# Performance work log

Hardware: AMD Instinct MI355X
Metric: run time of the kernel (lower is better)

Reference implementation:

```python
import jax, jax.numpy as jnp
import numpy as np

B, S, D = 4, 2048, 1024

def setup_inputs() -> dict:
    key = jax.random.key(0)
    k1, k2, k3, k4 = jax.random.split(key, 4)
    scale = 1.0 / np.sqrt(D)  # roughly glorot-like magnitude for weights
    return {
        "inputs": jax.random.normal(k1, (B, S, D), dtype=jnp.float32),
        "W_query": jax.random.normal(k2, (D, D), dtype=jnp.float32) * scale,
        "W_key": jax.random.normal(k3, (D, D), dtype=jnp.float32) * scale,
        "W_value": jax.random.normal(k4, (D, D), dtype=jnp.float32) * scale,
    }

def reference(inputs, W_query, W_key, W_value):
    # QKV projections: [B,S,D] @ [D,D]
    q = jnp.einsum('bsd,de->bse', inputs, W_query)
    k = jnp.einsum('bsd,de->bse', inputs, W_key)
    v = jnp.einsum('bsd,de->bse', inputs, W_value)
    # Unscaled attention scores [B,S,S] (source applies no 1/sqrt(d))
    score = jnp.einsum('bqd,bkd->bqk', q, k)
    weights = jax.nn.softmax(score, axis=-1)
    context = jnp.einsum('bqk,bkd->bqd', weights, v)
    return context
```

## Files before the change

### kernel.cpp

```cpp
#include <hip/hip_runtime.h>
#include <math.h>


typedef __bf16 bf16;
typedef _Float16 f16;
typedef __bf16 bf16x8 __attribute__((ext_vector_type(8)));
typedef __bf16 bf16x4 __attribute__((ext_vector_type(4)));
typedef _Float16 f16x4 __attribute__((ext_vector_type(4)));
typedef _Float16 f16x8 __attribute__((ext_vector_type(8)));
typedef float  f32x4  __attribute__((ext_vector_type(4)));

template<typename E> struct vec8_of;
template<> struct vec8_of<bf16> { using type = bf16x8; };
template<> struct vec8_of<f16>  { using type = f16x8; };

__device__ inline f32x4 mfma16(bf16x8 a, bf16x8 b, f32x4 c) {
    return __builtin_amdgcn_mfma_f32_16x16x32_bf16(a, b, c, 0, 0, 0);
}
__device__ inline f32x4 mfma16(f16x8 a, f16x8 b, f32x4 c) {
    return __builtin_amdgcn_mfma_f32_16x16x32_f16(a, b, c, 0, 0, 0);
}

#define AS1 __attribute__((address_space(1)))
#define AS3 __attribute__((address_space(3)))

template<typename E>
__device__ inline void async_load16(const E* g, void* l) {
    __builtin_amdgcn_global_load_lds((const AS1 unsigned int*)g,
                                     (AS3 unsigned int*)l, 16, 0, 0);
}

#define SBAR()  do { __builtin_amdgcn_s_barrier(); __builtin_amdgcn_sched_barrier(0); } while (0)
#define WAITV(n) do { asm volatile("s_waitcnt vmcnt(" #n ")" ::: "memory"); __builtin_amdgcn_sched_barrier(0); } while (0)
#define WAITL() do { asm volatile("s_waitcnt lgkmcnt(0)" ::: "memory"); __builtin_amdgcn_sched_barrier(0); } while (0)

__device__ inline void xcd_swz(int nwg, int gx, int& bx, int& by) {
    const int flat = by * gx + bx;
    const int s = (flat & 7) * (nwg >> 3) + (flat >> 3);
    bx = s % gx;
    by = s / gx;
}

template<int OUT_MODE, int BMQ>
__device__ __forceinline__ void gemm_deep_body(
    char* __restrict__ smraw,
    const f16* __restrict__ A, const f16* __restrict__ B,
    float* __restrict__ Cf, f16* __restrict__ Ch,
    int K, int lda, int ldb, int ldc,
    long long sA, long long sB, long long sC,
    int bx, int by, int bz)
{
    constexpr int ACH   = BMQ * 8192;
    constexpr int BOFF  = 2 * ACH;
    constexpr int BUFSZ = 2 * ACH + 32768;
    constexpr int nI    = 4 * BMQ;

    A += (long long)bz * sA;
    B += (long long)bz * sB;

    const int tid  = threadIdx.x;
    const int lane = tid & 63;
    const int wave = tid >> 6;
    const int quad = lane >> 4;
    const int l16  = lane & 15;
    const int wm   = wave >> 2;
    const int wn   = wave & 3;

    const long long rowA0 = (long long)by * (BMQ * 128);
    const long long colB0 = (long long)bx * 256;

    const int line0 = tid >> 3;
    const int slog  = (tid & 7) ^ (line0 & 7);
    const int r0s   = line0 * 2 + (slog >> 2);
    const int c0s   = (slog & 3) * 8;

    const f16* aSrc0 = A + (rowA0 + r0s) * lda + c0s;
    const f16* aSrc1 = A + (rowA0 + 128 + r0s) * lda + c0s;
    const f16* bSrc0 = B + (colB0 + r0s) * ldb + c0s;
    const f16* bSrc1 = B + (colB0 + 128 + r0s) * ldb + c0s;

    const int nt = K >> 6;

    auto stageA = [&](int t, int kh) {
        char* dst = smraw + (t & 1) * BUFSZ + kh * ACH;
        const int k0 = t * 64 + kh * 32;
        async_load16(aSrc0 + k0, dst + tid * 16);
        if constexpr (BMQ == 2) async_load16(aSrc1 + k0, dst + 8192 + tid * 16);
    };
    auto stageB = [&](int t, int kh) {
        char* dst = smraw + (t & 1) * BUFSZ + BOFF + kh * 16384;
        const int k0 = t * 64 + kh * 32;
        async_load16(bSrc0 + k0, dst + tid * 16);
        async_load16(bSrc1 + k0, dst + 8192 + tid * 16);
    };

    const int h    = l16 >> 1;
    const int lofs = h * 128 + ((((l16 & 1) * 4 + quad) ^ h) << 4);
    const int aoff = wm * (ACH / 2) + lofs;
    const int boff = BOFF + wn * 4096 + lofs;

    f32x4 acc[nI][4];
#pragma unroll
    for (int i = 0; i < nI; i++)
#pragma unroll
        for (int j = 0; j < 4; j++) acc[i][j] = (f32x4){0.f, 0.f, 0.f, 0.f};

    stageA(0, 0); stageA(0, 1); stageB(0, 0); stageB(0, 1);
    WAITV(2);
    SBAR();

    for (int t = 0; t < nt; t++) {
        const char* buf = smraw + (t & 1) * BUFSZ;
        f16x8 av[nI], bv[2];

#pragma unroll
        for (int i = 0; i < nI; i++) av[i] = *(const f16x8*)(buf + aoff + i * 1024);
        bv[0] = *(const f16x8*)(buf + boff);
        bv[1] = *(const f16x8*)(buf + boff + 1024);
        if (t + 1 < nt) { stageA(t + 1, 0); stageA(t + 1, 1); }
        SBAR();
        WAITL();
        __builtin_amdgcn_s_setprio(1);
#pragma unroll
        for (int i = 0; i < nI; i++) {
            acc[i][0] = mfma16(av[i], bv[0], acc[i][0]);
            acc[i][1] = mfma16(av[i], bv[1], acc[i][1]);
        }
        __builtin_amdgcn_s_setprio(0);
        SBAR();

        bv[0] = *(const f16x8*)(buf + boff + 2048);
        bv[1] = *(const f16x8*)(buf + boff + 3072);
        if (t + 1 < nt) { stageB(t + 1, 0); stageB(t + 1, 1); }
        SBAR();
        WAITL();
        __builtin_amdgcn_s_setprio(1);
#pragma unroll
        for (int i = 0; i < nI; i++) {
            acc[i][2] = mfma16(av[i], bv[0], acc[i][2]);
            acc[i][3] = mfma16(av[i], bv[1], acc[i][3]);
        }
        __builtin_amdgcn_s_setprio(0);
        if (t + 1 < nt) { if constexpr (BMQ == 2) WAITV(8); else WAITV(6); }
        else { WAITV(0); }
        SBAR();

#pragma unroll
        for (int i = 0; i < nI; i++) av[i] = *(const f16x8*)(buf + ACH + aoff + i * 1024);
        bv[0] = *(const f16x8*)(buf + 16384 + boff);
        bv[1] = *(const f16x8*)(buf + 16384 + boff + 1024);
        SBAR();
        WAITL();
        __builtin_amdgcn_s_setprio(1);
#pragma unroll
        for (int i = 0; i < nI; i++) {
            acc[i][0] = mfma16(av[i], bv[0], acc[i][0]);
            acc[i][1] = mfma16(av[i], bv[1], acc[i][1]);
        }
        __builtin_amdgcn_s_setprio(0);
        SBAR();

        bv[0] = *(const f16x8*)(buf + 16384 + boff + 2048);
        bv[1] = *(const f16x8*)(buf + 16384 + boff + 3072);
        SBAR();
        WAITL();
        __builtin_amdgcn_s_setprio(1);
#pragma unroll
        for (int i = 0; i < nI; i++) {
            acc[i][2] = mfma16(av[i], bv[0], acc[i][2]);
            acc[i][3] = mfma16(av[i], bv[1], acc[i][3]);
        }
        __builtin_amdgcn_s_setprio(0);
        if (t + 1 < nt) { WAITV(2); } else { WAITV(0); }
        SBAR();
    }

    if constexpr (OUT_MODE == 2) {
        auto tr = (f16(*)[72])smraw;
        const int batch = (int)(rowA0 >> 11);
        const long long rib = rowA0 & 2047;
        const int c  = tid >> 1;
        const int r0 = (tid & 1) << 5;
#pragma unroll
        for (int h2 = 0; h2 < 2; h2++)
#pragma unroll
            for (int iq = 0; iq < 2; iq++) {
                __syncthreads();
                if (wm == h2) {
#pragma unroll
                    for (int i2 = 0; i2 < 4; i2++)
#pragma unroll
                        for (int j = 0; j < 4; j++)
#pragma unroll
                            for (int e = 0; e < 4; e++)
                                tr[wn * 64 + j * 16 + l16][i2 * 16 + quad * 4 + e] =
                                    (f16)acc[iq * 4 + i2][j][e];
                }
                __syncthreads();
                f16* vt = Ch + (long long)batch * 1024 * 2048 +
                          (long long)(colB0 + c) * ldc + rib + h2 * 128 + iq * 64 + r0;
#pragma unroll
                for (int u = 0; u < 32; u += 8)
                    *(f16x8*)(vt + u) = *(const f16x8*)&tr[c][r0 + u];
            }
        return;
    }

    const long long cOff = (long long)bz * sC +
                           (rowA0 + wm * (BMQ * 64) + quad * 4) * (long long)ldc +
                           colB0 + wn * 64 + l16;
#pragma unroll
    for (int i = 0; i < nI; i++)
#pragma unroll
        for (int e = 0; e < 4; e++) {
            const long long ro = cOff + (long long)(i * 16 + e) * ldc;
            if (OUT_MODE == 0) {
                float* rp = Cf + ro;
#pragma unroll
                for (int j = 0; j < 4; j++) rp[j * 16] = acc[i][j][e];
            } else {
                f16* rp = Ch + ro;
#pragma unroll
                for (int j = 0; j < 4; j++) rp[j * 16] = (f16)acc[i][j][e];
            }
        }
}

__global__ __launch_bounds__(512, 2) void tv8d(
    const f16* __restrict__ Xf, const f16* __restrict__ Mt_f,
    const f16* __restrict__ Wvt_f, f16* __restrict__ T, f16* __restrict__ Vt)
{
    extern __shared__ char smraw[];
    int bx = blockIdx.x, by = blockIdx.y;
    xcd_swz(256, 8, bx, by);
    if (bx < 4)
        gemm_deep_body<1, 2>(smraw, Xf, Mt_f, nullptr, T, 1024, 1024, 1024, 1024,
                             0, 0, 0, bx, by, 0);
    else
        gemm_deep_body<2, 2>(smraw, Xf, Wvt_f, nullptr, Vt, 1024, 1024, 1024, 2048,
                             0, 0, 0, bx - 4, by, 0);
}

template<int OUT_MODE, int BMQ>
__global__ __launch_bounds__(512, 2) void gemmd_k(
    const f16* __restrict__ A, const f16* __restrict__ B,
    float* __restrict__ Cf, f16* __restrict__ Ch,
    int K, int lda, int ldb, int ldc,
    long long sA, long long sB, long long sC)
{
    extern __shared__ char smraw[];
    int bx = blockIdx.x, by = blockIdx.y;
    xcd_swz(gridDim.x * gridDim.y, gridDim.x, bx, by);
    gemm_deep_body<OUT_MODE, BMQ>(smraw, A, B, Cf, Ch, K, lda, ldb, ldc,
                                  sA, sB, sC, bx, by, blockIdx.z);
}

template<int OUT_MODE, int BMQ>
__device__ __forceinline__ void gemm8_body(
    char* __restrict__ smraw,
    const f16* __restrict__ A, const f16* __restrict__ B,
    float* __restrict__ Cf, f16* __restrict__ Ch,
    int K, int lda, int ldb, int ldc,
    long long sA, long long sB, long long sC,
    int bx, int by, int bz)
{
    constexpr int B0OFF = BMQ * 8192;
    constexpr int B1OFF = B0OFF + 8192;
    constexpr int BUFSZ = B0OFF + 16384;

    A += (long long)bz * sA;
    B += (long long)bz * sB;

    const int tid  = threadIdx.x;
    const int lane = tid & 63;
    const int wave = tid >> 6;
    const int quad = lane >> 4;
    const int l16  = lane & 15;
    const int wm   = wave >> 2;
    const int wn   = wave & 3;

    const long long rowA0 = (long long)by * (BMQ * 128);
    const long long colB0 = (long long)bx * 256;

    const int line0 = tid >> 3;
    const int slog  = (tid & 7) ^ (line0 & 7);
    const int aRow0 = line0 * 2 + (slog >> 2);
    const int aCol0 = (slog & 3) * 8;
    const int bRow  = ((aRow0 >> 5) << 6) + (aRow0 & 31);

    const f16* aSrc0 = A + (rowA0 + aRow0) * lda + aCol0;
    const f16* aSrc1 = A + (rowA0 + 128 + aRow0) * lda + aCol0;
    const f16* b0Src = B + (colB0 + bRow) * ldb + aCol0;
    const f16* b1Src = b0Src + 32LL * ldb;

    const int dA0 = tid * 16, dA1 = 8192 + tid * 16;

    const int nt = K >> 5;

    auto stageA = [&](int t) {
        char* buf = smraw + (t & 1) * BUFSZ;
        async_load16(aSrc0 + t * 32, buf + dA0);
        if (BMQ == 2) async_load16(aSrc1 + t * 32, buf + dA1);
    };
    auto stageB0 = [&](int t) {
        char* buf = smraw + (t & 1) * BUFSZ;
        async_load16(b0Src + t * 32, buf + B0OFF + dA0);
    };
    auto stageB1 = [&](int t) {
        char* buf = smraw + (t & 1) * BUFSZ;
        async_load16(b1Src + t * 32, buf + B1OFF + dA0);
    };

    const int h    = l16 >> 1;
    const int lofs = h * 128 + ((((l16 & 1) * 4 + quad) ^ h) << 4);
    const int aoff = wm * (BMQ * 4096) + lofs;
    const int boff = wn * 2048 + lofs;

    f32x4 acc[4 * BMQ][4];
#pragma unroll
    for (int i = 0; i < 4 * BMQ; i++)
#pragma unroll
        for (int j = 0; j < 4; j++) acc[i][j] = (f32x4){0.f, 0.f, 0.f, 0.f};

    stageA(0); stageB0(0); stageB1(0);
    stageA(1); stageB0(1);
    if constexpr (BMQ == 2) WAITV(4); else WAITV(3);
    SBAR();

    for (int t = 0; t < nt; t++) {
        const char* buf = smraw + (t & 1) * BUFSZ;
        f16x8 av[4 * BMQ], bv[2];

#pragma unroll
        for (int i = 0; i < 4 * BMQ; i++) av[i] = *(const f16x8*)(buf + aoff + i * 1024);
#pragma unroll
        for (int j = 0; j < 2; j++) bv[j] = *(const f16x8*)(buf + B0OFF + boff + j * 1024);
        if (t + 1 < nt) stageB1(t + 1);
        SBAR();
        WAITL();
        __builtin_amdgcn_s_setprio(1);
#pragma unroll
        for (int i = 0; i < 4 * BMQ; i++) {
            acc[i][0] = mfma16(av[i], bv[0], acc[i][0]);
            acc[i][1] = mfma16(av[i], bv[1], acc[i][1]);
        }
        __builtin_amdgcn_s_setprio(0);
        if (t + 1 < nt) { if constexpr (BMQ == 2) WAITV(4); else WAITV(3); }
        else WAITV(0);
        SBAR();

#pragma unroll
        for (int j = 0; j < 2; j++) bv[j] = *(const f16x8*)(buf + B1OFF + boff + j * 1024);
        if (t + 2 < nt) { stageA(t + 2); stageB0(t + 2); }
        SBAR();
        WAITL();
        __builtin_amdgcn_s_setprio(1);
#pragma unroll
        for (int i = 0; i < 4 * BMQ; i++) {
            acc[i][2] = mfma16(av[i], bv[0], acc[i][2]);
            acc[i][3] = mfma16(av[i], bv[1], acc[i][3]);
        }
        __builtin_amdgcn_s_setprio(0);
        if (t + 2 < nt) { if constexpr (BMQ == 2) WAITV(4); else WAITV(3); }
        else if (t + 1 < nt) WAITV(1);
        SBAR();
    }

    if constexpr (OUT_MODE == 2) {
        auto tr = (f16(*)[72])smraw;
        const int batch = (int)(rowA0 >> 11);
        const long long rib = rowA0 & 2047;
        const int c  = tid >> 1;
        const int r0 = (tid & 1) << 5;
#pragma unroll
        for (int h2 = 0; h2 < 2; h2++)
#pragma unroll
            for (int iq = 0; iq < 2; iq++) {
                __syncthreads();
                if (wm == h2) {
#pragma unroll
                    for (int i2 = 0; i2 < 4; i2++)
#pragma unroll
                        for (int j = 0; j < 4; j++)
#pragma unroll
                            for (int e = 0; e < 4; e++)
                                tr[wn * 64 + j * 16 + l16][i2 * 16 + quad * 4 + e] =
                                    (f16)acc[iq * 4 + i2][j][e];
                }
                __syncthreads();
                f16* vt = Ch + (long long)batch * 1024 * 2048 +
                          (long long)(colB0 + c) * ldc + rib + h2 * 128 + iq * 64 + r0;
#pragma unroll
                for (int u = 0; u < 32; u += 8)
                    *(f16x8*)(vt + u) = *(const f16x8*)&tr[c][r0 + u];
            }
        return;
    }

    const long long cOff = (long long)bz * sC +
                           (rowA0 + wm * (BMQ * 64) + quad * 4) * (long long)ldc +
                           colB0 + wn * 64 + l16;
#pragma unroll
    for (int i = 0; i < 4 * BMQ; i++)
#pragma unroll
        for (int e = 0; e < 4; e++) {
            const long long ro = cOff + (long long)(i * 16 + e) * ldc;
            if (OUT_MODE == 0) {
                float* rp = Cf + ro;
#pragma unroll
                for (int j = 0; j < 4; j++) rp[j * 16] = acc[i][j][e];
            } else {
                f16* rp = Ch + ro;
#pragma unroll
                for (int j = 0; j < 4; j++) rp[j * 16] = (f16)acc[i][j][e];
            }
        }
}

__global__ __launch_bounds__(512, 2) void tv8(
    const f16* __restrict__ Xf, const f16* __restrict__ Mt_f,
    const f16* __restrict__ Wvt_f, f16* __restrict__ T, f16* __restrict__ Vt)
{
    extern __shared__ char smraw[];
    int bx = blockIdx.x, by = blockIdx.y;
    xcd_swz(256, 8, bx, by);
    if (bx < 4)
        gemm8_body<1, 2>(smraw, Xf, Mt_f, nullptr, T, 1024, 1024, 1024, 1024,
                         0, 0, 0, bx, by, 0);
    else
        gemm8_body<2, 2>(smraw, Xf, Wvt_f, nullptr, Vt, 1024, 1024, 1024, 2048,
                         0, 0, 0, bx - 4, by, 0);
}

template<int OUT_MODE, int BMQ>
__global__ __launch_bounds__(512, 2) void gemm8_k(
    const f16* __restrict__ A, const f16* __restrict__ B,
    float* __restrict__ Cf, f16* __restrict__ Ch,
    int K, int lda, int ldb, int ldc,
    long long sA, long long sB, long long sC)
{
    extern __shared__ char smraw[];
    int bx = blockIdx.x, by = blockIdx.y;
    xcd_swz(gridDim.x * gridDim.y, gridDim.x, bx, by);
    gemm8_body<OUT_MODE, BMQ>(smraw, A, B, Cf, Ch, K, lda, ldb, ldc, sA, sB, sC,
                              bx, by, blockIdx.z);
}

template<typename E, bool SPLIT, int OUT_MODE, int BK>
__device__ __forceinline__ void gemm_body(
    char* __restrict__ smraw,
    const E* __restrict__ Ahi, const E* __restrict__ Alo,
    const E* __restrict__ Bhi, const E* __restrict__ Blo,
    float* __restrict__ Cf, f16* __restrict__ Ch,
    int K, int lda, int ldb, int ldc,
    long long sA, long long sB, long long sC,
    int bx, int by, int bz)
{
    using vec8 = typename vec8_of<E>::type;
    constexpr int TILE_BYTES = 128 * BK * (int)sizeof(E);
    constexpr int CPW = (TILE_BYTES / 1024) / 4;
    constexpr int SPR = (BK * (int)sizeof(E)) / 16;

    Ahi += (long long)bz * sA;
    Bhi += (long long)bz * sB;
    if (SPLIT) { Alo += (long long)bz * sA; Blo += (long long)bz * sB; }

    const int tid  = threadIdx.x;
    const int lane = tid & 63;
    const int wave = tid >> 6;
    const int quad = lane >> 4;
    const int l16  = lane & 15;
    const int wm   = (wave >> 1) * 64;
    const int wn   = (wave & 1) * 64;

    const long long rowA0 = (long long)by * 128;
    const long long colB0 = (long long)bx * 128;

    auto swz = [](int r) -> int { return (SPR == 8) ? (r & 7) : ((r >> 1) & 3); };

    int ofs[CPW], rr[CPW], cc8[CPW];
#pragma unroll
    for (int u = 0; u < CPW; u++) {
        ofs[u] = (wave * CPW + u) * 1024 + lane * 16;
        const int s = ofs[u] >> 4;
        rr[u]  = s / SPR;
        cc8[u] = (s & (SPR - 1)) ^ swz(rr[u]);
    }

    f32x4 acc[4][4];
#pragma unroll
    for (int i = 0; i < 4; i++)
#pragma unroll
        for (int j = 0; j < 4; j++) acc[i][j] = (f32x4){0.f, 0.f, 0.f, 0.f};

    for (int k0 = 0; k0 < K; k0 += BK) {
#pragma unroll
        for (int u = 0; u < CPW; u++) {
            async_load16(Ahi + (rowA0 + rr[u]) * lda + k0 + cc8[u] * 8, smraw + 0 * TILE_BYTES + ofs[u]);
            async_load16(Bhi + (colB0 + rr[u]) * ldb + k0 + cc8[u] * 8, smraw + 1 * TILE_BYTES + ofs[u]);
            if (SPLIT) {
                async_load16(Alo + (rowA0 + rr[u]) * lda + k0 + cc8[u] * 8, smraw + 2 * TILE_BYTES + ofs[u]);
                async_load16(Blo + (colB0 + rr[u]) * ldb + k0 + cc8[u] * 8, smraw + 3 * TILE_BYTES + ofs[u]);
            }
        }
        __syncthreads();

#pragma unroll
        for (int kh = 0; kh < BK / 32; kh++) {
            const int kc8 = kh * 4 + quad;
            vec8 a_hi[4], b_hi[4], a_lo[4], b_lo[4];
#pragma unroll
            for (int i = 0; i < 4; i++) {
                const int ra = wm + i * 16 + l16;
                const int rb = wn + i * 16 + l16;
                const int oa = ra * (SPR * 16) + ((kc8 ^ swz(ra)) << 4);
                const int ob = rb * (SPR * 16) + ((kc8 ^ swz(rb)) << 4);
                a_hi[i] = *(const vec8*)(smraw + 0 * TILE_BYTES + oa);
                b_hi[i] = *(const vec8*)(smraw + 1 * TILE_BYTES + ob);
                if (SPLIT) {
                    a_lo[i] = *(const vec8*)(smraw + 2 * TILE_BYTES + oa);
                    b_lo[i] = *(const vec8*)(smraw + 3 * TILE_BYTES + ob);
                }
            }
#pragma unroll
            for (int i = 0; i < 4; i++)
#pragma unroll
                for (int j = 0; j < 4; j++) {
                    acc[i][j] = mfma16(a_hi[i], b_hi[j], acc[i][j]);
                    if (SPLIT) {
                        acc[i][j] = mfma16(a_hi[i], b_lo[j], acc[i][j]);
                        acc[i][j] = mfma16(a_lo[i], b_hi[j], acc[i][j]);
                    }
                }
        }
        __syncthreads();
    }

    const long long cOff = (long long)bz * sC +
                           (rowA0 + wm + quad * 4) * (long long)ldc + colB0 + wn + l16;
#pragma unroll
    for (int i = 0; i < 4; i++)
#pragma unroll
        for (int e = 0; e < 4; e++) {
            const long long ro = cOff + (i * 16 + e) * ldc;
            if (OUT_MODE == 0) {
                float* rp = Cf + ro;
#pragma unroll
                for (int j = 0; j < 4; j++) rp[j * 16] = acc[i][j][e];
            } else {
                f16* rp = Ch + ro;
#pragma unroll
                for (int j = 0; j < 4; j++) rp[j * 16] = (f16)acc[i][j][e];
            }
        }
}

template<typename E, bool SPLIT, int OUT_MODE, int BK>
__global__ __launch_bounds__(256) void gemm_bt(
    const E* __restrict__ Ahi, const E* __restrict__ Alo,
    const E* __restrict__ Bhi, const E* __restrict__ Blo,
    float* __restrict__ Cf, f16* __restrict__ Ch,
    int K, int lda, int ldb, int ldc,
    long long sA, long long sB, long long sC)
{
    extern __shared__ char smraw[];
    gemm_body<E, SPLIT, OUT_MODE, BK>(smraw, Ahi, Alo, Bhi, Blo, Cf, Ch,
                                      K, lda, ldb, ldc, sA, sB, sC,
                                      blockIdx.x, blockIdx.y, blockIdx.z);
}

__global__ __launch_bounds__(256) void prep_all(
    const float4* __restrict__ X, f16* __restrict__ Xf,
    const float* __restrict__ Wq, const float* __restrict__ Wk, const float* __restrict__ Wv,
    bf16* __restrict__ Wq_h, bf16* __restrict__ Wq_l,
    bf16* __restrict__ Wk_h, bf16* __restrict__ Wk_l,
    f16* __restrict__ Wvt_f)
{
    int b = blockIdx.x;
    if (b < 8192) {
        long long i = (long long)b * 256 + threadIdx.x;
        float4 v = X[i];
        f16x4 fv = {(f16)v.x, (f16)v.y, (f16)v.z, (f16)v.w};
        *(f16x4*)(Xf + 4 * i) = fv;
    } else if (b < 10240) {
        const int b2 = b - 8192;
        const float4* W = (const float4*)(b2 < 1024 ? Wq : Wk);
        bf16* hh = b2 < 1024 ? Wq_h : Wk_h;
        bf16* ll = b2 < 1024 ? Wq_l : Wk_l;
        long long i = (long long)(b2 & 1023) * 256 + threadIdx.x;
        float4 v = W[i];
        bf16 a0 = (bf16)v.x, a1 = (bf16)v.y, a2 = (bf16)v.z, a3 = (bf16)v.w;
        bf16x4 hv = {a0, a1, a2, a3};
        bf16x4 lv = {(bf16)(v.x - (float)a0), (bf16)(v.y - (float)a1),
                     (bf16)(v.z - (float)a2), (bf16)(v.w - (float)a3)};
        *(bf16x4*)(hh + 4 * i) = hv;
        *(bf16x4*)(ll + 4 * i) = lv;
    } else {
        const int b3 = b - 10240;
        __shared__ float t[32][33];
        const int bx = (b3 & 31) * 32, by = (b3 >> 5) * 32;
        const int tx = threadIdx.x & 31, ty = threadIdx.x >> 5;
#pragma unroll
        for (int i = 0; i < 32; i += 8)
            t[ty + i][tx] = Wv[(long long)(by + ty + i) * 1024 + bx + tx];
        __syncthreads();
#pragma unroll
        for (int i = 0; i < 32; i += 8) {
            long long o = (long long)(bx + ty + i) * 1024 + by + tx;
            Wvt_f[o] = (f16)t[tx][ty + i];
        }
    }
}

__global__ __launch_bounds__(256) void softmax_f16(const float* __restrict__ S,
                                                   f16* __restrict__ P, int n)
{
    const long long row = blockIdx.x;
    const float4* p = (const float4*)(S + row * (long long)n);
    f16* q = P + row * (long long)n;
    const int tid = threadIdx.x;
    const int wv = tid >> 6, lane = tid & 63;

    float4 va = p[tid], vb = p[tid + 256];
    float v[8] = {va.x, va.y, va.z, va.w, vb.x, vb.y, vb.z, vb.w};
    float m = -3.4e38f;
#pragma unroll
    for (int i = 0; i < 8; i++) m = fmaxf(m, v[i]);
#pragma unroll
    for (int off = 32; off > 0; off >>= 1) m = fmaxf(m, __shfl_xor(m, off, 64));

    __shared__ float red[4];
    if (lane == 0) red[wv] = m;
    __syncthreads();
    m = fmaxf(fmaxf(red[0], red[1]), fmaxf(red[2], red[3]));

    float s = 0.f;
#pragma unroll
    for (int i = 0; i < 8; i++) { v[i] = __expf(v[i] - m); s += v[i]; }
#pragma unroll
    for (int off = 32; off > 0; off >>= 1) s += __shfl_xor(s, off, 64);
    __syncthreads();
    if (lane == 0) red[wv] = s;
    __syncthreads();
    s = red[0] + red[1] + red[2] + red[3];

    const float inv = 1.0f / s;
    f16x4 o0 = {(f16)(v[0] * inv), (f16)(v[1] * inv), (f16)(v[2] * inv), (f16)(v[3] * inv)};
    f16x4 o1 = {(f16)(v[4] * inv), (f16)(v[5] * inv), (f16)(v[6] * inv), (f16)(v[7] * inv)};
    *(f16x4*)(q + tid * 4) = o0;
    *(f16x4*)(q + 1024 + tid * 4) = o1;
}

extern "C" void kernel_launch(void* const* d_in, const int* in_sizes, int n_in,
                              void* d_out, int out_size, void* d_ws, size_t ws_size,
                              hipStream_t stream) {
    const float* X  = (const float*)d_in[0];
    const float* Wq = (const float*)d_in[1];
    const float* Wk = (const float*)d_in[2];
    const float* Wv = (const float*)d_in[3];
    float* out = (float*)d_out;

    char* w = (char*)d_ws;
    const long long MB = 1024LL * 1024;
    f16*  Xf    = (f16*) (w + 0 * MB);
    bf16* Wq_h  = (bf16*)(w + 16 * MB);
    bf16* Wq_l  = (bf16*)(w + 18 * MB);
    bf16* Wk_h  = (bf16*)(w + 20 * MB);
    bf16* Wk_l  = (bf16*)(w + 22 * MB);
    f16*  Wvt_f = (f16*) (w + 24 * MB);
    f16*  Mt_f  = (f16*) (w + 26 * MB);
    f16*  T     = (f16*) (w + 28 * MB);
    f16*  Vt    = (f16*) (w + 44 * MB);
    float* Sc   = (float*)(w + 60 * MB);
    f16*  P     = (f16*) (w + 124 * MB);

    static int deep_ok = -1;
    if (deep_ok < 0) {
        auto* pSc = gemmd_k<0, 2>;
        auto* pPv = gemmd_k<0, 1>;
        hipError_t e1 = hipFuncSetAttribute(
            reinterpret_cast<const void*>(tv8d),
            hipFuncAttributeMaxDynamicSharedMemorySize, 131072);
        hipError_t e2 = hipFuncSetAttribute(
            reinterpret_cast<const void*>(pSc),
            hipFuncAttributeMaxDynamicSharedMemorySize, 131072);
        hipError_t e3 = hipFuncSetAttribute(
            reinterpret_cast<const void*>(pPv),
            hipFuncAttributeMaxDynamicSharedMemorySize, 98304);
        deep_ok = (e1 == hipSuccess && e2 == hipSuccess && e3 == hipSuccess) ? 1 : 0;
    }

    dim3 blk(256);

    prep_all<<<dim3(11264), blk, 0, stream>>>(
        (const float4*)X, Xf, Wq, Wk, Wv, Wq_h, Wq_l, Wk_h, Wk_l, Wvt_f);

    gemm_bt<bf16, true, 1, 32><<<dim3(8, 8, 1), blk, 32768, stream>>>(
        Wk_h, Wk_l, Wq_h, Wq_l, nullptr, Mt_f,
        1024, 1024, 1024, 1024, 0, 0, 0);

    if (deep_ok) {
        tv8d<<<dim3(8, 32), dim3(512), 131072, stream>>>(Xf, Mt_f, Wvt_f, T, Vt);
        gemmd_k<0, 2><<<dim3(8, 8, 4), dim3(512), 131072, stream>>>(
            T, Xf, Sc, nullptr, 1024, 1024, 1024, 2048,
            2048LL * 1024, 2048LL * 1024, 2048LL * 2048);
        softmax_f16<<<dim3(4 * 2048), blk, 0, stream>>>(Sc, P, 2048);
        gemmd_k<0, 1><<<dim3(4, 16, 4), dim3(512), 98304, stream>>>(
            P, Vt, out, nullptr, 2048, 2048, 2048, 1024,
            2048LL * 2048, 1024LL * 2048, 2048LL * 1024);
    } else {
        tv8<<<dim3(8, 32), dim3(512), 65536, stream>>>(Xf, Mt_f, Wvt_f, T, Vt);
        gemm8_k<0, 2><<<dim3(8, 8, 4), dim3(512), 65536, stream>>>(
            T, Xf, Sc, nullptr, 1024, 1024, 1024, 2048,
            2048LL * 1024, 2048LL * 1024, 2048LL * 2048);
        softmax_f16<<<dim3(4 * 2048), blk, 0, stream>>>(Sc, P, 2048);
        gemm8_k<0, 1><<<dim3(4, 16, 4), dim3(512), 49152, stream>>>(
            P, Vt, out, nullptr, 2048, 2048, 2048, 1024,
            2048LL * 2048, 1024LL * 2048, 2048LL * 1024);
    }
}
```

Baseline: 275.2 us.

## Fuse whole attention pipeline into one cooperative persistent kernel with grid barriers

Replaces the chain of separate launches (prep, weight-product GEMM, projection GEMMs, score GEMM, softmax, PV GEMM) with a single cooperative kernel of 256 persistent blocks. The stages are separated by a software grid barrier built from an atomic counter. The aim is to remove per-launch overhead and the idle tail between kernels. In exchange it adds barrier spin cost and loses the per-kernel XCD swizzle. The small Mt GEMM is also computed redundantly by both 256-thread halves of each 512-thread block, and the unused gemm8 fallback path is removed.

```diff
diff --git a/kernel.cpp b/kernel.cpp
--- a/kernel.cpp
+++ b/kernel.cpp
@@ -39,6 +39,18 @@
     const int s = (flat & 7) * (nwg >> 3) + (flat >> 3);
     bx = s % gx;
     by = s / gx;
+}
+
+__device__ inline void gbar(unsigned* bar, unsigned target) {
+    __syncthreads();
+    if (threadIdx.x == 0) {
+        __threadfence();
+        atomicAdd(bar, 1u);
+        while (__hip_atomic_load(bar, __ATOMIC_RELAXED, __HIP_MEMORY_SCOPE_AGENT) < target)
+            __builtin_amdgcn_s_sleep(32);
+    }
+    __syncthreads();
+    __threadfence();
 }
 
 template<int OUT_MODE, int BMQ>
@@ -226,226 +238,6 @@
         }
 }
 
-__global__ __launch_bounds__(512, 2) void tv8d(
-    const f16* __restrict__ Xf, const f16* __restrict__ Mt_f,
-    const f16* __restrict__ Wvt_f, f16* __restrict__ T, f16* __restrict__ Vt)
-{
-    extern __shared__ char smraw[];
-    int bx = blockIdx.x, by = blockIdx.y;
-    xcd_swz(256, 8, bx, by);
-    if (bx < 4)
-        gemm_deep_body<1, 2>(smraw, Xf, Mt_f, nullptr, T, 1024, 1024, 1024, 1024,
-                             0, 0, 0, bx, by, 0);
-    else
-        gemm_deep_body<2, 2>(smraw, Xf, Wvt_f, nullptr, Vt, 1024, 1024, 1024, 2048,
-                             0, 0, 0, bx - 4, by, 0);
-}
-
-template<int OUT_MODE, int BMQ>
-__global__ __launch_bounds__(512, 2) void gemmd_k(
-    const f16* __restrict__ A, const f16* __restrict__ B,
-    float* __restrict__ Cf, f16* __restrict__ Ch,
-    int K, int lda, int ldb, int ldc,
-    long long sA, long long sB, long long sC)
-{
-    extern __shared__ char smraw[];
-    int bx = blockIdx.x, by = blockIdx.y;
-    xcd_swz(gridDim.x * gridDim.y, gridDim.x, bx, by);
-    gemm_deep_body<OUT_MODE, BMQ>(smraw, A, B, Cf, Ch, K, lda, ldb, ldc,
-                                  sA, sB, sC, bx, by, blockIdx.z);
-}
-
-template<int OUT_MODE, int BMQ>
-__device__ __forceinline__ void gemm8_body(
-    char* __restrict__ smraw,
-    const f16* __restrict__ A, const f16* __restrict__ B,
-    float* __restrict__ Cf, f16* __restrict__ Ch,
-    int K, int lda, int ldb, int ldc,
-    long long sA, long long sB, long long sC,
-    int bx, int by, int bz)
-{
-    constexpr int B0OFF = BMQ * 8192;
-    constexpr int B1OFF = B0OFF + 8192;
-    constexpr int BUFSZ = B0OFF + 16384;
-
-    A += (long long)bz * sA;
-    B += (long long)bz * sB;
-
-    const int tid  = threadIdx.x;
-    const int lane = tid & 63;
-    const int wave = tid >> 6;
-    const int quad = lane >> 4;
-    const int l16  = lane & 15;
-    const int wm   = wave >> 2;
-    const int wn   = wave & 3;
-
-    const long long rowA0 = (long long)by * (BMQ * 128);
-    const long long colB0 = (long long)bx * 256;
-
-    const int line0 = tid >> 3;
-    const int slog  = (tid & 7) ^ (line0 & 7);
-    const int aRow0 = line0 * 2 + (slog >> 2);
-    const int aCol0 = (slog & 3) * 8;
-    const int bRow  = ((aRow0 >> 5) << 6) + (aRow0 & 31);
-
-    const f16* aSrc0 = A + (rowA0 + aRow0) * lda + aCol0;
-    const f16* aSrc1 = A + (rowA0 + 128 + aRow0) * lda + aCol0;
-    const f16* b0Src = B + (colB0 + bRow) * ldb + aCol0;
-    const f16* b1Src = b0Src + 32LL * ldb;
-
-    const int dA0 = tid * 16, dA1 = 8192 + tid * 16;
-
-    const int nt = K >> 5;
-
-    auto stageA = [&](int t) {
-        char* buf = smraw + (t & 1) * BUFSZ;
-        async_load16(aSrc0 + t * 32, buf + dA0);
-        if (BMQ == 2) async_load16(aSrc1 + t * 32, buf + dA1);
-    };
-    auto stageB0 = [&](int t) {
-        char* buf = smraw + (t & 1) * BUFSZ;
-        async_load16(b0Src + t * 32, buf + B0OFF + dA0);
-    };
-    auto stageB1 = [&](int t) {
-        char* buf = smraw + (t & 1) * BUFSZ;
-        async_load16(b1Src + t * 32, buf + B1OFF + dA0);
-    };
-
-    const int h    = l16 >> 1;
-    const int lofs = h * 128 + ((((l16 & 1) * 4 + quad) ^ h) << 4);
-    const int aoff = wm * (BMQ * 4096) + lofs;
-    const int boff = wn * 2048 + lofs;
-
-    f32x4 acc[4 * BMQ][4];
-#pragma unroll
-    for (int i = 0; i < 4 * BMQ; i++)
-#pragma unroll
-        for (int j = 0; j < 4; j++) acc[i][j] = (f32x4){0.f, 0.f, 0.f, 0.f};
-
-    stageA(0); stageB0(0); stageB1(0);
-    stageA(1); stageB0(1);
-    if constexpr (BMQ == 2) WAITV(4); else WAITV(3);
-    SBAR();
-
-    for (int t = 0; t < nt; t++) {
-        const char* buf = smraw + (t & 1) * BUFSZ;
-        f16x8 av[4 * BMQ], bv[2];
-
-#pragma unroll
-        for (int i = 0; i < 4 * BMQ; i++) av[i] = *(const f16x8*)(buf + aoff + i * 1024);
-#pragma unroll
-        for (int j = 0; j < 2; j++) bv[j] = *(const f16x8*)(buf + B0OFF + boff + j * 1024);
-        if (t + 1 < nt) stageB1(t + 1);
-        SBAR();
-        WAITL();
-        __builtin_amdgcn_s_setprio(1);
-#pragma unroll
-        for (int i = 0; i < 4 * BMQ; i++) {
-            acc[i][0] = mfma16(av[i], bv[0], acc[i][0]);
-            acc[i][1] = mfma16(av[i], bv[1], acc[i][1]);
-        }
-        __builtin_amdgcn_s_setprio(0);
-        if (t + 1 < nt) { if constexpr (BMQ == 2) WAITV(4); else WAITV(3); }
-        else WAITV(0);
-        SBAR();
-
-#pragma unroll
-        for (int j = 0; j < 2; j++) bv[j] = *(const f16x8*)(buf + B1OFF + boff + j * 1024);
-        if (t + 2 < nt) { stageA(t + 2); stageB0(t + 2); }
-        SBAR();
-        WAITL();
-        __builtin_amdgcn_s_setprio(1);
-#pragma unroll
-        for (int i = 0; i < 4 * BMQ; i++) {
-            acc[i][2] = mfma16(av[i], bv[0], acc[i][2]);
-            acc[i][3] = mfma16(av[i], bv[1], acc[i][3]);
-        }
-        __builtin_amdgcn_s_setprio(0);
-        if (t + 2 < nt) { if constexpr (BMQ == 2) WAITV(4); else WAITV(3); }
-        else if (t + 1 < nt) WAITV(1);
-        SBAR();
-    }
-
-    if constexpr (OUT_MODE == 2) {
-        auto tr = (f16(*)[72])smraw;
-        const int batch = (int)(rowA0 >> 11);
-        const long long rib = rowA0 & 2047;
-        const int c  = tid >> 1;
-        const int r0 = (tid & 1) << 5;
-#pragma unroll
-        for (int h2 = 0; h2 < 2; h2++)
-#pragma unroll
-            for (int iq = 0; iq < 2; iq++) {
-                __syncthreads();
-                if (wm == h2) {
-#pragma unroll
-                    for (int i2 = 0; i2 < 4; i2++)
-#pragma unroll
-                        for (int j = 0; j < 4; j++)
-#pragma unroll
-                            for (int e = 0; e < 4; e++)
-                                tr[wn * 64 + j * 16 + l16][i2 * 16 + quad * 4 + e] =
-                                    (f16)acc[iq * 4 + i2][j][e];
-                }
-                __syncthreads();
-                f16* vt = Ch + (long long)batch * 1024 * 2048 +
-                          (long long)(colB0 + c) * ldc + rib + h2 * 128 + iq * 64 + r0;
-#pragma unroll
-                for (int u = 0; u < 32; u += 8)
-                    *(f16x8*)(vt + u) = *(const f16x8*)&tr[c][r0 + u];
-            }
-        return;
-    }
-
-    const long long cOff = (long long)bz * sC +
-                           (rowA0 + wm * (BMQ * 64) + quad * 4) * (long long)ldc +
-                           colB0 + wn * 64 + l16;
-#pragma unroll
-    for (int i = 0; i < 4 * BMQ; i++)
-#pragma unroll
-        for (int e = 0; e < 4; e++) {
-            const long long ro = cOff + (long long)(i * 16 + e) * ldc;
-            if (OUT_MODE == 0) {
-                float* rp = Cf + ro;
-#pragma unroll
-                for (int j = 0; j < 4; j++) rp[j * 16] = acc[i][j][e];
-            } else {
-                f16* rp = Ch + ro;
-#pragma unroll
-                for (int j = 0; j < 4; j++) rp[j * 16] = (f16)acc[i][j][e];
-            }
-        }
-}
-
-__global__ __launch_bounds__(512, 2) void tv8(
-    const f16* __restrict__ Xf, const f16* __restrict__ Mt_f,
-    const f16* __restrict__ Wvt_f, f16* __restrict__ T, f16* __restrict__ Vt)
-{
-    extern __shared__ char smraw[];
-    int bx = blockIdx.x, by = blockIdx.y;
-    xcd_swz(256, 8, bx, by);
-    if (bx < 4)
-        gemm8_body<1, 2>(smraw, Xf, Mt_f, nullptr, T, 1024, 1024, 1024, 1024,
-                         0, 0, 0, bx, by, 0);
-    else
-        gemm8_body<2, 2>(smraw, Xf, Wvt_f, nullptr, Vt, 1024, 1024, 1024, 2048,
-                         0, 0, 0, bx - 4, by, 0);
-}
-
-template<int OUT_MODE, int BMQ>
-__global__ __launch_bounds__(512, 2) void gemm8_k(
-    const f16* __restrict__ A, const f16* __restrict__ B,
-    float* __restrict__ Cf, f16* __restrict__ Ch,
-    int K, int lda, int ldb, int ldc,
-    long long sA, long long sB, long long sC)
-{
-    extern __shared__ char smraw[];
-    int bx = blockIdx.x, by = blockIdx.y;
-    xcd_swz(gridDim.x * gridDim.y, gridDim.x, bx, by);
-    gemm8_body<OUT_MODE, BMQ>(smraw, A, B, Cf, Ch, K, lda, ldb, ldc, sA, sB, sC,
-                              bx, by, blockIdx.z);
-}
-
 template<typename E, bool SPLIT, int OUT_MODE, int BK>
 __device__ __forceinline__ void gemm_body(
     char* __restrict__ smraw,
@@ -454,7 +246,7 @@
     float* __restrict__ Cf, f16* __restrict__ Ch,
     int K, int lda, int ldb, int ldc,
     long long sA, long long sB, long long sC,
-    int bx, int by, int bz)
+    int bx, int by, int bz, int tid)
 {
     using vec8 = typename vec8_of<E>::type;
     constexpr int TILE_BYTES = 128 * BK * (int)sizeof(E);
@@ -465,7 +257,6 @@
     Bhi += (long long)bz * sB;
     if (SPLIT) { Alo += (long long)bz * sA; Blo += (long long)bz * sB; }
 
-    const int tid  = threadIdx.x;
     const int lane = tid & 63;
     const int wave = tid >> 6;
     const int quad = lane >> 4;
@@ -555,6 +346,162 @@
         }
 }
 
+__device__ __forceinline__ void softmax512(const float* __restrict__ S,
+                                           f16* __restrict__ P,
+                                           long long row, int tid, char* smraw)
+{
+    float* red = (float*)smraw;
+    const float4* p = (const float4*)(S + row * 2048);
+    f16* q = P + row * 2048;
+    const int wv = tid >> 6, lane = tid & 63;
+
+    float4 va = p[tid];
+    float m = fmaxf(fmaxf(va.x, va.y), fmaxf(va.z, va.w));
+#pragma unroll
+    for (int off = 32; off > 0; off >>= 1) m = fmaxf(m, __shfl_xor(m, off, 64));
+    __syncthreads();
+    if (lane == 0) red[wv] = m;
+    __syncthreads();
+    m = fmaxf(fmaxf(fmaxf(red[0], red[1]), fmaxf(red[2], red[3])),
+              fmaxf(fmaxf(red[4], red[5]), fmaxf(red[6], red[7])));
+
+    float e0 = __expf(va.x - m), e1 = __expf(va.y - m);
+    float e2 = __expf(va.z - m), e3 = __expf(va.w - m);
+    float s = (e0 + e1) + (e2 + e3);
+#pragma unroll
+    for (int off = 32; off > 0; off >>= 1) s += __shfl_xor(s, off, 64);
+    __syncthreads();
+    if (lane == 0) red[wv] = s;
+    __syncthreads();
+    s = ((red[0] + red[1]) + (red[2] + red[3])) +
+        ((red[4] + red[5]) + (red[6] + red[7]));
+
+    const float inv = 1.0f / s;
+    f16x4 o = {(f16)(e0 * inv), (f16)(e1 * inv), (f16)(e2 * inv), (f16)(e3 * inv)};
+    *(f16x4*)(q + tid * 4) = o;
+}
+
+__global__ __launch_bounds__(512, 2) void mega(
+    const float* __restrict__ X, const float* __restrict__ Wq,
+    const float* __restrict__ Wk, const float* __restrict__ Wv,
+    float* __restrict__ out, f16* __restrict__ Xf,
+    bf16* __restrict__ Wq_h, bf16* __restrict__ Wq_l,
+    bf16* __restrict__ Wk_h, bf16* __restrict__ Wk_l,
+    f16* __restrict__ Wvt_f, f16* __restrict__ Mt_f,
+    f16* __restrict__ T, f16* __restrict__ Vt,
+    float* __restrict__ Sc, f16* __restrict__ P, unsigned* bar)
+{
+    extern __shared__ char smraw[];
+    const int b = blockIdx.x, tid = threadIdx.x;
+
+    for (int u = b; u < 1536; u += 256) {
+        if (u < 1024) {
+            const float4* W = (const float4*)(u < 512 ? Wq : Wk);
+            bf16* hh = u < 512 ? Wq_h : Wk_h;
+            bf16* ll = u < 512 ? Wq_l : Wk_l;
+            long long i = (long long)(u & 511) * 512 + tid;
+            float4 v = W[i];
+            bf16 a0 = (bf16)v.x, a1 = (bf16)v.y, a2 = (bf16)v.z, a3 = (bf16)v.w;
+            bf16x4 hv = {a0, a1, a2, a3};
+            bf16x4 lv = {(bf16)(v.x - (float)a0), (bf16)(v.y - (float)a1),
+                         (bf16)(v.z - (float)a2), (bf16)(v.w - (float)a3)};
+            *(bf16x4*)(hh + 4 * i) = hv;
+            *(bf16x4*)(ll + 4 * i) = lv;
+        } else {
+            auto t = (float(*)[32][33])smraw;
+            const int tile = (u - 1024) * 2 + (tid >> 8);
+            const int sub = tid & 255;
+            const int bx = (tile & 31) * 32, by = (tile >> 5) * 32;
+            const int tx = sub & 31, ty = sub >> 5;
+            __syncthreads();
+#pragma unroll
+            for (int i = 0; i < 32; i += 8)
+                t[tid >> 8][ty + i][tx] = Wv[(long long)(by + ty + i) * 1024 + bx + tx];
+            __syncthreads();
+#pragma unroll
+            for (int i = 0; i < 32; i += 8) {
+                long long o = (long long)(bx + ty + i) * 1024 + by + tx;
+                Wvt_f[o] = (f16)t[tid >> 8][tx][ty + i];
+            }
+        }
+    }
+    gbar(bar, 256);
+
+    if (b < 64) {
+        gemm_body<bf16, true, 1, 32>(smraw, Wk_h, Wk_l, Wq_h, Wq_l,
+                                     nullptr, Mt_f, 1024, 1024, 1024, 1024,
+                                     0, 0, 0, b & 7, b >> 3, 0, tid & 255);
+    } else {
+        for (int u = b - 64; u < 4096; u += 192) {
+            long long i = (long long)u * 512 + tid;
+            float4 v = ((const float4*)X)[i];
+            f16x4 fv = {(f16)v.x, (f16)v.y, (f16)v.z, (f16)v.w};
+            *(f16x4*)(Xf + 4 * i) = fv;
+        }
+    }
+    gbar(bar, 512);
+
+    if (b < 128) {
+        const int by = (b & 7) * 4 + ((b >> 3) & 3), bx = b >> 5;
+        gemm_deep_body<1, 2>(smraw, Xf, Mt_f, nullptr, T, 1024, 1024, 1024, 1024,
+                             0, 0, 0, bx, by, 0);
+    } else {
+        const int b2 = b - 128;
+        const int by = (b2 & 7) * 4 + ((b2 >> 3) & 3), bx = b2 >> 5;
+        gemm_deep_body<2, 2>(smraw, Xf, Wvt_f, nullptr, Vt, 1024, 1024, 1024, 2048,
+                             0, 0, 0, bx, by, 0);
+    }
+    gbar(bar, 768);
+
+    {
+        const int rem = b & 63, bz = b >> 6;
+        const int by = rem & 7, bx = rem >> 3;
+        gemm_deep_body<0, 2>(smraw, T, Xf, Sc, nullptr, 1024, 1024, 1024, 2048,
+                             2048LL * 1024, 2048LL * 1024, 2048LL * 2048, bx, by, bz);
+    }
+    gbar(bar, 1024);
+
+    for (int r = 0; r < 32; r++)
+        softmax512(Sc, P, (long long)b * 32 + r, tid, smraw);
+    gbar(bar, 1280);
+
+    {
+        const int rem = b & 63, bz = b >> 6;
+        const int by = (rem & 7) * 2 + ((rem >> 3) & 1), bx = rem >> 4;
+        gemm_deep_body<0, 1>(smraw, P, Vt, out, nullptr, 2048, 2048, 2048, 1024,
+                             2048LL * 2048, 1024LL * 2048, 2048LL * 1024, bx, by, bz);
+    }
+}
+
+__global__ __launch_bounds__(512, 2) void tv8d(
+    const f16* __restrict__ Xf, const f16* __restrict__ Mt_f,
+    const f16* __restrict__ Wvt_f, f16* __restrict__ T, f16* __restrict__ Vt)
+{
+    extern __shared__ char smraw[];
+    int bx = blockIdx.x, by = blockIdx.y;
+    xcd_swz(256, 8, bx, by);
+    if (bx < 4)
+        gemm_deep_body<1, 2>(smraw, Xf, Mt_f, nullptr, T, 1024, 1024, 1024, 1024,
+                             0, 0, 0, bx, by, 0);
+    else
+        gemm_deep_body<2, 2>(smraw, Xf, Wvt_f, nullptr, Vt, 1024, 1024, 1024, 2048,
+                             0, 0, 0, bx - 4, by, 0);
+}
+
+template<int OUT_MODE, int BMQ>
+__global__ __launch_bounds__(512, 2) void gemmd_k(
+    const f16* __restrict__ A, const f16* __restrict__ B,
+    float* __restrict__ Cf, f16* __restrict__ Ch,
+    int K, int lda, int ldb, int ldc,
+    long long sA, long long sB, long long sC)
+{
+    extern __shared__ char smraw[];
+    int bx = blockIdx.x, by = blockIdx.y;
+    xcd_swz(gridDim.x * gridDim.y, gridDim.x, bx, by);
+    gemm_deep_body<OUT_MODE, BMQ>(smraw, A, B, Cf, Ch, K, lda, ldb, ldc,
+                                  sA, sB, sC, bx, by, blockIdx.z);
+}
+
 template<typename E, bool SPLIT, int OUT_MODE, int BK>
 __global__ __launch_bounds__(256) void gemm_bt(
     const E* __restrict__ Ahi, const E* __restrict__ Alo,
@@ -566,7 +513,8 @@
     extern __shared__ char smraw[];
     gemm_body<E, SPLIT, OUT_MODE, BK>(smraw, Ahi, Alo, Bhi, Blo, Cf, Ch,
                                       K, lda, ldb, ldc, sA, sB, sC,
-                                      blockIdx.x, blockIdx.y, blockIdx.z);
+                                      blockIdx.x, blockIdx.y, blockIdx.z,
+                                      threadIdx.x);
 }
 
 __global__ __launch_bounds__(256) void prep_all(
@@ -674,10 +622,13 @@
     float* Sc   = (float*)(w + 60 * MB);
     f16*  P     = (f16*) (w + 124 * MB);
 
-    static int deep_ok = -1;
-    if (deep_ok < 0) {
+    static int attrs_ok = -1;
+    if (attrs_ok < 0) {
         auto* pSc = gemmd_k<0, 2>;
         auto* pPv = gemmd_k<0, 1>;
+        hipError_t e0 = hipFuncSetAttribute(
+            reinterpret_cast<const void*>(mega),
+            hipFuncAttributeMaxDynamicSharedMemorySize, 131072);
         hipError_t e1 = hipFuncSetAttribute(
             reinterpret_cast<const void*>(tv8d),
             hipFuncAttributeMaxDynamicSharedMemorySize, 131072);
@@ -687,19 +638,31 @@
         hipError_t e3 = hipFuncSetAttribute(
             reinterpret_cast<const void*>(pPv),
             hipFuncAttributeMaxDynamicSharedMemorySize, 98304);
-        deep_ok = (e1 == hipSuccess && e2 == hipSuccess && e3 == hipSuccess) ? 1 : 0;
+        attrs_ok = ((e1 == hipSuccess && e2 == hipSuccess && e3 == hipSuccess) ? 1 : 0)
+                 | ((e0 == hipSuccess) ? 2 : 0);
+    }
+
+    if ((attrs_ok & 2) && ws_size >= (size_t)(156 * MB + 64)) {
+        unsigned* bar = (unsigned*)(w + 156 * MB);
+        hipMemsetAsync(bar, 0, 4, stream);
+        void* kargs[] = { (void*)&X, (void*)&Wq, (void*)&Wk, (void*)&Wv,
+                          (void*)&out, (void*)&Xf,
+                          (void*)&Wq_h, (void*)&Wq_l, (void*)&Wk_h, (void*)&Wk_l,
+                          (void*)&Wvt_f, (void*)&Mt_f, (void*)&T, (void*)&Vt,
+                          (void*)&Sc, (void*)&P, (void*)&bar };
+        hipError_t err = hipLaunchCooperativeKernel(
+            reinterpret_cast<void*>(mega), dim3(256), dim3(512), kargs,
+            131072, stream);
+        if (err == hipSuccess) return;
     }
 
     dim3 blk(256);
-
     prep_all<<<dim3(11264), blk, 0, stream>>>(
         (const float4*)X, Xf, Wq, Wk, Wv, Wq_h, Wq_l, Wk_h, Wk_l, Wvt_f);
-
     gemm_bt<bf16, true, 1, 32><<<dim3(8, 8, 1), blk, 32768, stream>>>(
         Wk_h, Wk_l, Wq_h, Wq_l, nullptr, Mt_f,
         1024, 1024, 1024, 1024, 0, 0, 0);
-
-    if (deep_ok) {
+    if (attrs_ok & 1) {
         tv8d<<<dim3(8, 32), dim3(512), 131072, stream>>>(Xf, Mt_f, Wvt_f, T, Vt);
         gemmd_k<0, 2><<<dim3(8, 8, 4), dim3(512), 131072, stream>>>(
             T, Xf, Sc, nullptr, 1024, 1024, 1024, 2048,
@@ -708,14 +671,5 @@
         gemmd_k<0, 1><<<dim3(4, 16, 4), dim3(512), 98304, stream>>>(
             P, Vt, out, nullptr, 2048, 2048, 2048, 1024,
             2048LL * 2048, 1024LL * 2048, 2048LL * 1024);
-    } else {
-        tv8<<<dim3(8, 32), dim3(512), 65536, stream>>>(Xf, Mt_f, Wvt_f, T, Vt);
-        gemm8_k<0, 2><<<dim3(8, 8, 4), dim3(512), 65536, stream>>>(
-            T, Xf, Sc, nullptr, 1024, 1024, 1024, 2048,
-            2048LL * 1024, 2048LL * 1024, 2048LL * 2048);
-        softmax_f16<<<dim3(4 * 2048), blk, 0, stream>>>(Sc, P, 2048);
-        gemm8_k<0, 1><<<dim3(4, 16, 4), dim3(512), 49152, stream>>>(
-            P, Vt, out, nullptr, 2048, 2048, 2048, 1024,
-            2048LL * 2048, 1024LL * 2048, 2048LL * 1024);
-    }
-}
+    }
+}
```

Result: slower. 570.8 us (+107.5%).
